# Kernel optimization log

Measured on AMD Instinct MI355X. Metric: run time of the kernel, lower is better.

Reference implementation:

```python
import jax, jax.numpy as jnp
import numpy as np

B, L, H, D, HID = 2, 2048, 16, 64, 1024
NB = 4  # n_branches


def setup_inputs() -> dict:
    key = jax.random.key(0)
    ks = jax.random.split(key, 10)
    gate_in = HID + 3 * D * NB + D * NB  # 2048
    return {
        "hidden": jax.random.normal(ks[0], (B, L, HID), jnp.float32),
        "branch0": jax.random.normal(ks[1], (B, L, H, D), jnp.float32),
        "branch1": jax.random.normal(ks[2], (B, L, H, D), jnp.float32),
        "branch2": jax.random.normal(ks[3], (B, L, H, D), jnp.float32),
        "branch3": jax.random.normal(ks[4], (B, L, H, D), jnp.float32),
        "W1": jax.random.normal(ks[5], (gate_in, 2 * D), jnp.float32) * 0.02,
        "b1": jnp.zeros((2 * D,), jnp.float32),
        "W2": jax.random.normal(ks[6], (2 * D, NB), jnp.float32) * 0.1,
        "b2": jnp.zeros((NB,), jnp.float32),
        "eps_floor": jax.random.uniform(ks[7], (H, NB), jnp.float32) * 0.02,
        "temp": jnp.ones((H,), jnp.float32),
    }


def _stat_feats(x):
    # x: [B,L,H,D] -> [B,L,H,3D] with (mean, rms, max) each broadcast over D
    mean = jnp.mean(x, axis=-1, keepdims=True)
    rms = jnp.sqrt(jnp.clip(jnp.mean(x * x, axis=-1, keepdims=True), 1e-8))
    maxv = jnp.max(x, axis=-1, keepdims=True)
    d = x.shape[-1]
    bc = lambda s: jnp.broadcast_to(s, x.shape[:-1] + (d,))
    return jnp.concatenate([bc(mean), bc(rms), bc(maxv)], axis=-1)


def reference(hidden, branch0, branch1, branch2, branch3, W1, b1, W2, b2, eps_floor, temp):
    branches = [branch0, branch1, branch2, branch3]
    stats = [_stat_feats(p) for p in branches]  # each [B,L,H,3D]
    hid_bc = jnp.broadcast_to(hidden[:, :, None, :], (B, L, H, HID))
    head_in = jnp.concatenate([hid_bc, *stats, *branches], axis=-1)  # [B,L,H,gate_in]
    h1 = jax.nn.gelu(jnp.einsum("blhi,io->blho", head_in, W1) + b1, approximate=False)
    logits = jnp.einsum("blho,on->blhn", h1, W2) + b2  # [B,L,H,4]
    t = jnp.clip(temp, 0.2, 10.0)[None, None, :, None]
    w = jax.nn.softmax(logits / t, axis=-1)
    floor = jnp.clip(eps_floor, 1e-7, 0.1)[None, None, :, :]
    w = jnp.maximum(w, floor)
    w = w / jnp.sum(w, axis=-1, keepdims=True)
    return w  # [B,L,H,4]
```

## Files before the change

kernel.cpp:

```cpp
#include <hip/hip_runtime.h>
#include <hip/hip_bf16.h>
#include <math.h>

#define NBL   4096
#define NPOS  65536
#define TWO_D 128
#define HIDN  1024

typedef __attribute__((ext_vector_type(8))) short short8;
typedef __attribute__((ext_vector_type(4))) float f32x4;
typedef __attribute__((ext_vector_type(4))) unsigned int uint4v;

__device__ inline short f2bf(float f) {
    union { float f; unsigned u; } v; v.f = f;
    unsigned r = (v.u + 0x7FFFu + ((v.u >> 16) & 1u)) >> 16;
    return (short)r;
}
__device__ inline unsigned pkbf(float x, float y) {
    __hip_bfloat162 h = __float22bfloat162_rn(make_float2(x, y));
    union { __hip_bfloat162 h; unsigned u; } c; c.h = h;
    return c.u;
}
__device__ inline float gelu_fast(float x) {
    const float x2 = x * x;
    const float u  = x * fmaf(x2, 0.044715f, 1.0f) * 1.5957691216057308f;
    const float e  = __expf(-u);
    return x * __builtin_amdgcn_rcpf(1.0f + e);
}


__global__ __launch_bounds__(256) void k_prep(const float* __restrict__ W1,
                                              short* __restrict__ WhS,
                                              short* __restrict__ WbT,
                                              short* __restrict__ wsT) {
    __shared__ float lds[16][129];
    __shared__ float acc2[128];
    const int b = blockIdx.x, t = threadIdx.x;
    if (b < 80) {
        int srcRow0; short* dst; int kofs;
        if (b < 64) {
            srcRow0 = b * 16;
            const int q = b >> 4;
            dst  = WhS + q * (128 * 256);
            kofs = (b * 16) & 255;
        } else {
            srcRow0 = 1792 + (b - 64) * 16;
            dst  = WbT;
            kofs = (b - 64) * 16;
        }
        #pragma unroll
        for (int i = 0; i < 8; ++i) {
            const int idx = i * 256 + t;
            const int row = idx >> 7, col = idx & 127;
            lds[row][col] = W1[(size_t)(srcRow0 + row) * TWO_D + col];
        }
        __syncthreads();
        #pragma unroll
        for (int i = 0; i < 8; ++i) {
            const int idx = i * 256 + t;
            const int n = idx >> 4, k = idx & 15;
            dst[(size_t)n * 256 + kofs + k] = f2bf(lds[k][n]);
        }
    } else {
        const int i = b - 80;
        const int j = i / 3, sx = i - 3 * j;
        const int base = HIDN + j * 192 + sx * 64;
        const int n = t & 127, dh = t >> 7;
        float s = 0.f;
        for (int d = 0; d < 32; ++d)
            s += W1[(size_t)(base + dh * 32 + d) * TWO_D + n];
        if (dh) acc2[n] = s;
        __syncthreads();
        if (!dh) {
            wsT[n * 32 + i] = f2bf(s + acc2[n]);
            if (i == 0)
                for (int p = 12; p < 32; ++p) wsT[n * 32 + p] = (short)0;
        }
    }
}

__global__ __launch_bounds__(256) void k_hid(const float* __restrict__ hidden,
                                             const short* __restrict__ WhS,
                                             float* __restrict__ hP) {
    __shared__ short wb[128 * 264];
    const int t    = threadIdx.x;
    const int lane = t & 63;
    const int w    = __builtin_amdgcn_readfirstlane(t >> 6);
    const int quad = lane >> 4, lm = lane & 15;
    const int q    = blockIdx.x & 3;
    const int mg   = blockIdx.x >> 2;
    const int r0   = (mg * 4 + w) * 16;

    const short* __restrict__ src = WhS + (size_t)q * (128 * 256);
    #pragma unroll
    for (int i = 0; i < 16; ++i) {
        const int idx = i * 256 + t;
        const int row = idx >> 5, col = (idx & 31) * 8;
        *(short8*)(wb + row * 264 + col) = *(const short8*)(src + row * 256 + col);
    }
    __syncthreads();

    f32x4 acc[8];
    #pragma unroll
    for (int nt = 0; nt < 8; ++nt) acc[nt] = (f32x4){0.f, 0.f, 0.f, 0.f};

    #pragma unroll
    for (int kk = 0; kk < 8; ++kk) {
        const int kc = kk * 32 + quad * 8;
        const int kG = q * 256 + kc;
        const float4 x0 = *(const float4*)(hidden + (size_t)(r0 + lm) * HIDN + kG);
        const float4 x1 = *(const float4*)(hidden + (size_t)(r0 + lm) * HIDN + kG + 4);
        union { short8 s; uint4v u; } a;
        a.u = (uint4v){pkbf(x0.x, x0.y), pkbf(x0.z, x0.w),
                       pkbf(x1.x, x1.y), pkbf(x1.z, x1.w)};
        #pragma unroll
        for (int nt = 0; nt < 8; ++nt) {
            const short8 bfr = *(const short8*)(wb + (nt * 16 + lm) * 264 + kc);
            acc[nt] = __builtin_amdgcn_mfma_f32_16x16x32_bf16(a.s, bfr, acc[nt], 0, 0, 0);
        }
    }

    float* __restrict__ dst = hP + (size_t)q * NBL * TWO_D;
    #pragma unroll
    for (int nt = 0; nt < 8; ++nt)
        #pragma unroll
        for (int r = 0; r < 4; ++r)
            dst[(size_t)(r0 + quad * 4 + r) * TWO_D + nt * 16 + lm] = acc[nt][r];
}

__global__ __launch_bounds__(512, 4) void k_main(
    const float* __restrict__ g0, const float* __restrict__ g1,
    const float* __restrict__ g2, const float* __restrict__ g3,
    const short* __restrict__ WbT, const short* __restrict__ wsT,
    const float* __restrict__ b1, const float* __restrict__ W2,
    const float* __restrict__ b2, const float* __restrict__ eps_floor,
    const float* __restrict__ temp, const float* __restrict__ hP,
    float* __restrict__ out) {

    __shared__ short wb[128 * 264];
    __shared__ float w2s[512];
    __shared__ float b1s[128];

    const int t    = threadIdx.x;
    const int lane = t & 63;
    const int w    = __builtin_amdgcn_readfirstlane(t >> 6);
    const int quad = lane >> 4, lm = lane & 15;
    const int bl   = blockIdx.x * 8 + w;
    const int pos0 = bl * 16;

    #pragma unroll
    for (int i = 0; i < 8; ++i) {
        const int idx = i * 512 + t;
        const int row = idx >> 5, col = (idx & 31) * 8;
        *(short8*)(wb + row * 264 + col) = *(const short8*)(WbT + row * 256 + col);
    }
    w2s[t] = W2[t];
    if (t < 128) b1s[t] = b1[t];
    __syncthreads();

    f32x4 acc[8];
    #pragma unroll
    for (int nt = 0; nt < 8; ++nt) acc[nt] = (f32x4){0.f, 0.f, 0.f, 0.f};

    float stm[12];
    const float* const bjs[4] = {g0, g1, g2, g3};
    #pragma unroll
    for (int j = 0; j < 4; ++j) {
        const float* __restrict__ bj = bjs[j];
        float s = 0.f, sq = 0.f, mx = -INFINITY;
        #pragma unroll
        for (int half = 0; half < 2; ++half) {
            const int kc = half * 32 + quad * 8;
            const float4 x0 = *(const float4*)(bj + (size_t)(pos0 + lm) * 64 + kc);
            const float4 x1 = *(const float4*)(bj + (size_t)(pos0 + lm) * 64 + kc + 4);
            s  += x0.x + x0.y + x0.z + x0.w + x1.x + x1.y + x1.z + x1.w;
            sq  = fmaf(x0.x, x0.x, sq); sq = fmaf(x0.y, x0.y, sq);
            sq  = fmaf(x0.z, x0.z, sq); sq = fmaf(x0.w, x0.w, sq);
            sq  = fmaf(x1.x, x1.x, sq); sq = fmaf(x1.y, x1.y, sq);
            sq  = fmaf(x1.z, x1.z, sq); sq = fmaf(x1.w, x1.w, sq);
            mx  = fmaxf(mx, fmaxf(fmaxf(x0.x, x0.y), fmaxf(x0.z, x0.w)));
            mx  = fmaxf(mx, fmaxf(fmaxf(x1.x, x1.y), fmaxf(x1.z, x1.w)));
            union { short8 s; uint4v u; } a;
            a.u = (uint4v){pkbf(x0.x, x0.y), pkbf(x0.z, x0.w),
                           pkbf(x1.x, x1.y), pkbf(x1.z, x1.w)};
            const int kg = j * 64 + half * 32 + quad * 8;
            #pragma unroll
            for (int nt = 0; nt < 8; ++nt) {
                const short8 bfr = *(const short8*)(wb + (nt * 16 + lm) * 264 + kg);
                acc[nt] = __builtin_amdgcn_mfma_f32_16x16x32_bf16(a.s, bfr, acc[nt], 0, 0, 0);
            }
        }
        float ss = s, qq = sq, mm = mx;
        ss += __shfl_xor(ss, 16); ss += __shfl_xor(ss, 32);
        qq += __shfl_xor(qq, 16); qq += __shfl_xor(qq, 32);
        mm  = fmaxf(mm, __shfl_xor(mm, 16)); mm = fmaxf(mm, __shfl_xor(mm, 32));
        stm[3 * j + 0] = ss * (1.f / 64.f);
        stm[3 * j + 1] = sqrtf(fmaxf(qq * (1.f / 64.f), 1e-8f));
        stm[3 * j + 2] = mm;
    }

    {
        short8 sa;
        #pragma unroll
        for (int jj = 0; jj < 8; ++jj) {
            float v;
            if (jj < 4) v = (quad == 0) ? stm[jj] : ((quad == 1) ? stm[8 + jj] : 0.f);
            else        v = (quad == 0) ? stm[jj] : 0.f;
            sa[jj] = f2bf(v);
        }
        #pragma unroll
        for (int nt = 0; nt < 8; ++nt) {
            const short8 bfr = *(const short8*)(wsT + (size_t)(nt * 16 + lm) * 32 + quad * 8);
            acc[nt] = __builtin_amdgcn_mfma_f32_16x16x32_bf16(sa, bfr, acc[nt], 0, 0, 0);
        }
    }

    const float4 b2v = *(const float4*)b2;
    float tcl[4]; float4 efl[4];
    #pragma unroll
    for (int r = 0; r < 4; ++r) {
        const int h = quad * 4 + r;
        tcl[r] = fminf(fmaxf(temp[h], 0.2f), 10.0f);
        efl[r] = *(const float4*)(eps_floor + h * 4);
    }

    float p[4][4];
    #pragma unroll
    for (int r = 0; r < 4; ++r)
        #pragma unroll
        for (int c = 0; c < 4; ++c) p[r][c] = 0.f;

    #pragma unroll
    for (int nt = 0; nt < 8; ++nt) {
        const int n = nt * 16 + lm;
        const size_t hi = (size_t)bl * TWO_D + n;
        const float hv = hP[hi] + hP[524288 + hi] + hP[2 * 524288 + hi]
                       + hP[3 * 524288 + hi];
        const float b1v = b1s[n];
        const float4 w2v = *(const float4*)(w2s + n * 4);
        #pragma unroll
        for (int r = 0; r < 4; ++r) {
            const float x = acc[nt][r] + hv + b1v;
            const float g = gelu_fast(x);
            p[r][0] = fmaf(g, w2v.x, p[r][0]);
            p[r][1] = fmaf(g, w2v.y, p[r][1]);
            p[r][2] = fmaf(g, w2v.z, p[r][2]);
            p[r][3] = fmaf(g, w2v.w, p[r][3]);
        }
    }
    #pragma unroll
    for (int r = 0; r < 4; ++r)
        #pragma unroll
        for (int c = 0; c < 4; ++c) {
            float v = p[r][c];
            v += __shfl_xor(v, 1); v += __shfl_xor(v, 2);
            v += __shfl_xor(v, 4); v += __shfl_xor(v, 8);
            p[r][c] = v;
        }

    #pragma unroll
    for (int r = 0; r < 4; ++r) {
        const float l0 = p[r][0] + b2v.x;
        const float l1 = p[r][1] + b2v.y;
        const float l2 = p[r][2] + b2v.z;
        const float l3 = p[r][3] + b2v.w;
        const float inv = 1.0f / tcl[r];
        const float m = fmaxf(fmaxf(l0, l1), fmaxf(l2, l3));
        float e0 = __expf((l0 - m) * inv);
        float e1 = __expf((l1 - m) * inv);
        float e2 = __expf((l2 - m) * inv);
        float e3 = __expf((l3 - m) * inv);
        const float rsum = 1.0f / (e0 + e1 + e2 + e3);
        float w0 = e0 * rsum, w1 = e1 * rsum, w2 = e2 * rsum, w3 = e3 * rsum;
        w0 = fmaxf(w0, fminf(fmaxf(efl[r].x, 1e-7f), 0.1f));
        w1 = fmaxf(w1, fminf(fmaxf(efl[r].y, 1e-7f), 0.1f));
        w2 = fmaxf(w2, fminf(fmaxf(efl[r].z, 1e-7f), 0.1f));
        w3 = fmaxf(w3, fminf(fmaxf(efl[r].w, 1e-7f), 0.1f));
        const float rs = 1.0f / (w0 + w1 + w2 + w3);
        if (lm == 0) {
            const int pos = pos0 + quad * 4 + r;
            float4 ov; ov.x = w0 * rs; ov.y = w1 * rs; ov.z = w2 * rs; ov.w = w3 * rs;
            *(float4*)(out + (size_t)pos * 4) = ov;
        }
    }
}

extern "C" void kernel_launch(void* const* d_in, const int* in_sizes, int n_in,
                              void* d_out, int out_size, void* d_ws, size_t ws_size,
                              hipStream_t stream) {
    const float* hidden = (const float*)d_in[0];
    const float* br0    = (const float*)d_in[1];
    const float* br1    = (const float*)d_in[2];
    const float* br2    = (const float*)d_in[3];
    const float* br3    = (const float*)d_in[4];
    const float* W1     = (const float*)d_in[5];
    const float* b1     = (const float*)d_in[6];
    const float* W2     = (const float*)d_in[7];
    const float* b2     = (const float*)d_in[8];
    const float* eps    = (const float*)d_in[9];
    const float* temp   = (const float*)d_in[10];
    float* out = (float*)d_out;

    char* wsb = (char*)d_ws;
    float* hP  = (float*)(wsb);
    short* WhS = (short*)(wsb + 8388608);
    short* WbT = (short*)(wsb + 8650752);
    short* wsT = (short*)(wsb + 8716288);

    hipLaunchKernelGGL(k_prep, dim3(92),  dim3(256), 0, stream, W1, WhS, WbT, wsT);
    hipLaunchKernelGGL(k_hid,  dim3(256), dim3(256), 0, stream, hidden, WhS, hP);
    hipLaunchKernelGGL(k_main, dim3(512), dim3(512), 0, stream,
                       br0, br1, br2, br3, WbT, wsT, b1, W2, b2, eps, temp,
                       hP, out);
}
```

Measured before the change: 137.8 us.

## Fold weight prep into consumer kernels and split hidden GEMM eight ways along K

Removes the separate k_prep launch. The W1 transpose and bf16 conversion now happen inside k_hid and k_main while each block loads its own LDS tile. k_hid splits K into 8 chunks of 128, so it launches 512 GEMM blocks plus 12 stat-sum blocks, and k_main reduces the 8 partial sums into shared memory once per block. This cuts one launch and raises parallelism in the hidden GEMM. In exchange, every block re-reads and converts W1 from fp32, and the partial-sum buffer doubles in size, which adds memory traffic.

Result: no change. 138.5 us (+0.5%).

```diff
diff --git a/kernel.cpp b/kernel.cpp
--- a/kernel.cpp
+++ b/kernel.cpp
@@ -8,6 +8,7 @@
 #define HIDN  1024
 
 typedef __attribute__((ext_vector_type(8))) short short8;
+typedef __attribute__((ext_vector_type(4))) short short4v;
 typedef __attribute__((ext_vector_type(4))) float f32x4;
 typedef __attribute__((ext_vector_type(4))) unsigned int uint4v;
 
@@ -29,40 +30,16 @@
 }
 
 
-__global__ __launch_bounds__(256) void k_prep(const float* __restrict__ W1,
-                                              short* __restrict__ WhS,
-                                              short* __restrict__ WbT,
-                                              short* __restrict__ wsT) {
-    __shared__ float lds[16][129];
+__global__ __launch_bounds__(256, 4) void k_hid(const float* __restrict__ hidden,
+                                                const float* __restrict__ W1,
+                                                float* __restrict__ hP,
+                                                short* __restrict__ wsT) {
+    __shared__ short wbh[128 * 136];
     __shared__ float acc2[128];
     const int b = blockIdx.x, t = threadIdx.x;
-    if (b < 80) {
-        int srcRow0; short* dst; int kofs;
-        if (b < 64) {
-            srcRow0 = b * 16;
-            const int q = b >> 4;
-            dst  = WhS + q * (128 * 256);
-            kofs = (b * 16) & 255;
-        } else {
-            srcRow0 = 1792 + (b - 64) * 16;
-            dst  = WbT;
-            kofs = (b - 64) * 16;
-        }
-        #pragma unroll
-        for (int i = 0; i < 8; ++i) {
-            const int idx = i * 256 + t;
-            const int row = idx >> 7, col = idx & 127;
-            lds[row][col] = W1[(size_t)(srcRow0 + row) * TWO_D + col];
-        }
-        __syncthreads();
-        #pragma unroll
-        for (int i = 0; i < 8; ++i) {
-            const int idx = i * 256 + t;
-            const int n = idx >> 4, k = idx & 15;
-            dst[(size_t)n * 256 + kofs + k] = f2bf(lds[k][n]);
-        }
-    } else {
-        const int i = b - 80;
+
+    if (b >= 512) {
+        const int i = b - 512;
         const int j = i / 3, sx = i - 3 * j;
         const int base = HIDN + j * 192 + sx * 64;
         const int n = t & 127, dh = t >> 7;
@@ -76,38 +53,41 @@
             if (i == 0)
                 for (int p = 12; p < 32; ++p) wsT[n * 32 + p] = (short)0;
         }
-    }
-}
-
-__global__ __launch_bounds__(256) void k_hid(const float* __restrict__ hidden,
-                                             const short* __restrict__ WhS,
-                                             float* __restrict__ hP) {
-    __shared__ short wb[128 * 264];
-    const int t    = threadIdx.x;
+        return;
+    }
+
+    const int ks   = b >> 6;
+    const int mg   = b & 63;
     const int lane = t & 63;
     const int w    = __builtin_amdgcn_readfirstlane(t >> 6);
     const int quad = lane >> 4, lm = lane & 15;
-    const int q    = blockIdx.x & 3;
-    const int mg   = blockIdx.x >> 2;
-    const int r0   = (mg * 4 + w) * 16;
-
-    const short* __restrict__ src = WhS + (size_t)q * (128 * 256);
-    #pragma unroll
-    for (int i = 0; i < 16; ++i) {
-        const int idx = i * 256 + t;
-        const int row = idx >> 5, col = (idx & 31) * 8;
-        *(short8*)(wb + row * 264 + col) = *(const short8*)(src + row * 256 + col);
+
+    {
+        const int n = t & 127, g = t >> 7;
+        #pragma unroll
+        for (int i = 0; i < 16; ++i) {
+            const int kb = i * 8 + g * 4;
+            const float v0 = W1[(size_t)(ks * 128 + kb + 0) * TWO_D + n];
+            const float v1 = W1[(size_t)(ks * 128 + kb + 1) * TWO_D + n];
+            const float v2 = W1[(size_t)(ks * 128 + kb + 2) * TWO_D + n];
+            const float v3 = W1[(size_t)(ks * 128 + kb + 3) * TWO_D + n];
+            union { short4v s; unsigned u[2]; } pk;
+            pk.u[0] = pkbf(v0, v1);
+            pk.u[1] = pkbf(v2, v3);
+            *(short4v*)(wbh + n * 136 + kb) = pk.s;
+        }
     }
     __syncthreads();
 
+    const int r0 = (mg * 4 + w) * 16;
     f32x4 acc[8];
     #pragma unroll
     for (int nt = 0; nt < 8; ++nt) acc[nt] = (f32x4){0.f, 0.f, 0.f, 0.f};
 
     #pragma unroll
-    for (int kk = 0; kk < 8; ++kk) {
-        const int kc = kk * 32 + quad * 8;
-        const int kG = q * 256 + kc;
+    for (int kk = 0; kk < 4; ++kk) {
+        const int kl = kk * 32 + quad * 8;
+        const int kG = ks * 128 + kl;
         const float4 x0 = *(const float4*)(hidden + (size_t)(r0 + lm) * HIDN + kG);
         const float4 x1 = *(const float4*)(hidden + (size_t)(r0 + lm) * HIDN + kG + 4);
         union { short8 s; uint4v u; } a;
@@ -115,12 +95,12 @@
                        pkbf(x1.x, x1.y), pkbf(x1.z, x1.w)};
         #pragma unroll
         for (int nt = 0; nt < 8; ++nt) {
-            const short8 bfr = *(const short8*)(wb + (nt * 16 + lm) * 264 + kc);
+            const short8 bfr = *(const short8*)(wbh + (nt * 16 + lm) * 136 + kl);
             acc[nt] = __builtin_amdgcn_mfma_f32_16x16x32_bf16(a.s, bfr, acc[nt], 0, 0, 0);
         }
     }
 
-    float* __restrict__ dst = hP + (size_t)q * NBL * TWO_D;
+    float* __restrict__ dst = hP + (size_t)ks * NBL * TWO_D;
     #pragma unroll
     for (int nt = 0; nt < 8; ++nt)
         #pragma unroll
@@ -131,13 +111,14 @@
 __global__ __launch_bounds__(512, 4) void k_main(
     const float* __restrict__ g0, const float* __restrict__ g1,
     const float* __restrict__ g2, const float* __restrict__ g3,
-    const short* __restrict__ WbT, const short* __restrict__ wsT,
+    const float* __restrict__ W1, const short* __restrict__ wsT,
     const float* __restrict__ b1, const float* __restrict__ W2,
     const float* __restrict__ b2, const float* __restrict__ eps_floor,
     const float* __restrict__ temp, const float* __restrict__ hP,
     float* __restrict__ out) {
 
     __shared__ short wb[128 * 264];
+    __shared__ float hids[1024];
     __shared__ float w2s[512];
     __shared__ float b1s[128];
 
@@ -148,11 +129,30 @@
     const int bl   = blockIdx.x * 8 + w;
     const int pos0 = bl * 16;
 
-    #pragma unroll
-    for (int i = 0; i < 8; ++i) {
-        const int idx = i * 512 + t;
-        const int row = idx >> 5, col = (idx & 31) * 8;
-        *(short8*)(wb + row * 264 + col) = *(const short8*)(WbT + row * 256 + col);
+    {
+        const int n = t & 127, g = t >> 7;
+        #pragma unroll
+        for (int i = 0; i < 16; ++i) {
+            const int kb = i * 16 + g * 4;
+            const float v0 = W1[(size_t)(1792 + kb + 0) * TWO_D + n];
+            const float v1 = W1[(size_t)(1792 + kb + 1) * TWO_D + n];
+            const float v2 = W1[(size_t)(1792 + kb + 2) * TWO_D + n];
+            const float v3 = W1[(size_t)(1792 + kb + 3) * TWO_D + n];
+            union { short4v s; unsigned u[2]; } pk;
+            pk.u[0] = pkbf(v0, v1);
+            pk.u[1] = pkbf(v2, v3);
+            *(short4v*)(wb + n * 264 + kb) = pk.s;
+        }
+    }
+    #pragma unroll
+    for (int e = 0; e < 2; ++e) {
+        const int idx = e * 512 + t;
+        const int bll = idx >> 7, nn = idx & 127;
+        const size_t base = (size_t)(blockIdx.x * 8 + bll) * TWO_D + nn;
+        float hv = 0.f;
+        #pragma unroll
+        for (int s = 0; s < 8; ++s) hv += hP[(size_t)s * 524288 + base];
+        hids[bll * 128 + nn] = hv;
     }
     w2s[t] = W2[t];
     if (t < 128) b1s[t] = b1[t];
@@ -233,9 +233,7 @@
     #pragma unroll
     for (int nt = 0; nt < 8; ++nt) {
         const int n = nt * 16 + lm;
-        const size_t hi = (size_t)bl * TWO_D + n;
-        const float hv = hP[hi] + hP[524288 + hi] + hP[2 * 524288 + hi]
-                       + hP[3 * 524288 + hi];
+        const float hv  = hids[w * 128 + n];
         const float b1v = b1s[n];
         const float4 w2v = *(const float4*)(w2s + n * 4);
         #pragma unroll
@@ -303,13 +301,10 @@
 
     char* wsb = (char*)d_ws;
     float* hP  = (float*)(wsb);
-    short* WhS = (short*)(wsb + 8388608);
-    short* WbT = (short*)(wsb + 8650752);
-    short* wsT = (short*)(wsb + 8716288);
-
-    hipLaunchKernelGGL(k_prep, dim3(92),  dim3(256), 0, stream, W1, WhS, WbT, wsT);
-    hipLaunchKernelGGL(k_hid,  dim3(256), dim3(256), 0, stream, hidden, WhS, hP);
+    short* wsT = (short*)(wsb + 16777216);
+
+    hipLaunchKernelGGL(k_hid,  dim3(524), dim3(256), 0, stream, hidden, W1, hP, wsT);
     hipLaunchKernelGGL(k_main, dim3(512), dim3(512), 0, stream,
-                       br0, br1, br2, br3, WbT, wsT, b1, W2, b2, eps, temp,
+                       br0, br1, br2, br3, W1, wsT, b1, W2, b2, eps, temp,
                        hP, out);
 }
```
